# Kernel optimization log

Hardware: AMD Instinct MI355X
Metric: run time of the kernel (lower is better)

Reference implementation:

```python
import jax, jax.numpy as jnp
import numpy as np

B, CTX, DIMS, HEAD = 8, 4096, 1024, 16
HD = DIMS // HEAD
EPS = 1e-5
THRESH = 0.01   # self.threshold.item()
FACTOR = 0.1    # self.factor.item()
MAX_IT = 3


def setup_inputs() -> dict:
    key = jax.random.key(0)
    ks = jax.random.split(key, 9)
    w = lambda k, shp: jax.random.normal(k, shp, jnp.float32) * 0.02
    return {
        "x": jax.random.normal(ks[0], (B, CTX, DIMS), jnp.float32),
        "qw": w(ks[1], (DIMS, DIMS)), "qb": jnp.zeros((DIMS,), jnp.float32),
        "kw": w(ks[2], (DIMS, DIMS)),  # k linear has bias=False
        "vw": w(ks[3], (DIMS, DIMS)), "vb": jnp.zeros((DIMS,), jnp.float32),
        "ow": w(ks[4], (DIMS, DIMS)), "ob": jnp.zeros((DIMS,), jnp.float32),
        "lna_w": jnp.ones((DIMS,), jnp.float32),
        "lnb_w": jnp.ones((DIMS,), jnp.float32),
        "lnc_w": jnp.ones((HD,), jnp.float32),
        "lnd_w": jnp.ones((HD,), jnp.float32),
        "lqw": w(ks[5], (HD, HD)), "lqb": jnp.zeros((HD,), jnp.float32),
        "lkw": w(ks[6], (HD, HD)), "lkb": jnp.zeros((HD,), jnp.float32),
        "lvw": w(ks[7], (HD, HD)), "lvb": jnp.zeros((HD,), jnp.float32),
    }


def _ln(x, w):
    # torch LayerNorm with bias=False (biased variance)
    m = jnp.mean(x, axis=-1, keepdims=True)
    v = jnp.mean((x - m) ** 2, axis=-1, keepdims=True)
    return (x - m) * jax.lax.rsqrt(v + EPS) * w


def reference(x, qw, qb, kw, vw, vb, ow, ob, lna_w, lnb_w, lnc_w, lnd_w,
              lqw, lqb, lkw, lkb, lvw, lvb):
    b, ctx, dims = x.shape
    q = _ln(x, lna_w) @ qw.T + qb
    xb = _ln(x, lnb_w)
    k = xb @ kw.T
    v = xb @ vw.T + vb
    split = lambda t: t.reshape(b, ctx, HEAD, HD).transpose(0, 2, 1, 3)  # [b,h,s,d]
    query, key_t, value = split(q), split(k), split(v)

    # Faithful to source bug: eff_span = min(seq, qcur.size(1)=head, key.size(1)=head)
    eff = min(ctx, HEAD)

    # key/value side of the inner loop is iteration-invariant -> compute once
    kn = _ln(key_t[:, :, :eff, :] @ lkw.T + lkb, lnd_w)
    vi = value[:, :, :eff, :] @ lvw.T + lvb
    scale = 1.0 / np.sqrt(HD)

    def step(qcur):
        qn = _ln(qcur[:, :, :eff, :] @ lqw.T + lqb, lnc_w)
        logits = jnp.einsum('bhqd,bhkd->bhqk', qn, kn) * scale
        attn = jax.nn.softmax(logits, axis=-1) @ vi  # is_causal=False (mask is None)
        return jnp.zeros_like(qcur).at[:, :, :eff, :].set(attn)

    prev = jnp.zeros_like(query)
    attn_out = jnp.zeros_like(query)
    qcur = query
    done = jnp.asarray(False)
    for it in range(MAX_IT):
        iter_out = step(qcur)
        diff = jnp.mean(jnp.abs(iter_out - prev))
        brk = (diff < THRESH + FACTOR * diff) & jnp.asarray(it > 0) & (~done)
        attn_out = jnp.where(done, attn_out, iter_out)
        prev = jnp.where(done, prev, iter_out)
        qcur = jnp.where(done | brk, qcur, qcur + iter_out)
        done = done | brk

    out = attn_out.transpose(0, 2, 1, 3).reshape(b, ctx, dims)
    return out @ ow.T + ob
```

## Files before the change

kernel.cpp:

```cpp
#include <hip/hip_runtime.h>

typedef unsigned short u16;
typedef __attribute__((ext_vector_type(8))) short short8;
typedef __attribute__((ext_vector_type(4))) float f32x4;

#define LSTR 68

__device__ __forceinline__ u16 f2bf(float f){
  union { float f; unsigned int i; } v; v.f = f;
  unsigned int x = v.i;
  return (u16)((x + 0x7FFFu + ((x >> 16) & 1u)) >> 16);
}

__device__ __forceinline__ short8 cvt8(const float* __restrict__ p){
  float4 a = *(const float4*)p;
  float4 b = *(const float4*)(p + 4);
  short8 r;
  r[0]=(short)f2bf(a.x); r[1]=(short)f2bf(a.y); r[2]=(short)f2bf(a.z); r[3]=(short)f2bf(a.w);
  r[4]=(short)f2bf(b.x); r[5]=(short)f2bf(b.y); r[6]=(short)f2bf(b.z); r[7]=(short)f2bf(b.w);
  return r;
}

__global__ __launch_bounds__(256) void k_ln(const float* __restrict__ x,
    const float* __restrict__ lna, const float* __restrict__ lnb,
    u16* __restrict__ xa, u16* __restrict__ xb)
{
  __shared__ float ssum[4], ssq[4];
  int row = blockIdx.x;
  int b = row >> 4, s = row & 15;
  int tid = threadIdx.x;
  const float* xr = x + ((size_t)b*4096 + s)*1024;
  float4 v = *(const float4*)(xr + tid*4);
  float sum = v.x+v.y+v.z+v.w;
  float sq  = v.x*v.x+v.y*v.y+v.z*v.z+v.w*v.w;
  #pragma unroll
  for (int o=32;o>0;o>>=1){ sum += __shfl_xor(sum,o); sq += __shfl_xor(sq,o); }
  int w = tid>>6;
  if ((tid&63)==0){ ssum[w]=sum; ssq[w]=sq; }
  __syncthreads();
  sum = ssum[0]+ssum[1]+ssum[2]+ssum[3];
  sq  = ssq[0]+ssq[1]+ssq[2]+ssq[3];
  float m   = sum * (1.f/1024.f);
  float var = sq  * (1.f/1024.f) - m*m;
  float rs  = rsqrtf(fmaxf(var, 0.f) + 1e-5f);
  float4 wa = *(const float4*)(lna + tid*4);
  float4 wb = *(const float4*)(lnb + tid*4);
  float n0=(v.x-m)*rs, n1=(v.y-m)*rs, n2=(v.z-m)*rs, n3=(v.w-m)*rs;
  ushort4 oa, obv;
  oa.x=f2bf(n0*wa.x); oa.y=f2bf(n1*wa.y); oa.z=f2bf(n2*wa.z); oa.w=f2bf(n3*wa.w);
  obv.x=f2bf(n0*wb.x); obv.y=f2bf(n1*wb.y); obv.z=f2bf(n2*wb.z); obv.w=f2bf(n3*wb.w);
  *(ushort4*)(xa + (size_t)row*1024 + tid*4) = oa;
  *(ushort4*)(xb + (size_t)row*1024 + tid*4) = obv;
}

__global__ __launch_bounds__(256) void k_proj(const u16* __restrict__ xa, const u16* __restrict__ xb,
    const float* __restrict__ qw, const float* __restrict__ qb,
    const float* __restrict__ kw, const float* __restrict__ vw, const float* __restrict__ vb,
    float* __restrict__ qkv)
{
  int tid = threadIdx.x, wave = tid>>6, lane = tid&63;
  int tile = blockIdx.x*4 + wave;
  int mt = tile / 192, nt = tile % 192;
  int mat = nt >> 6, nct = nt & 63;
  const u16*   A = (mat==0) ? xa : xb;
  const float* W = (mat==0) ? qw : ((mat==1) ? kw : vw);
  int m_lane = lane & 15, quad = lane >> 4;
  const u16*   ap = A + (size_t)(mt*16  + m_lane)*1024 + quad*8;
  const float* bp = W + (size_t)(nct*16 + m_lane)*1024 + quad*8;
  f32x4 acc = {0.f,0.f,0.f,0.f};
  #pragma unroll 4
  for (int k0=0;k0<1024;k0+=32){
    short8 af = *(const short8*)(ap + k0);
    short8 bf = cvt8(bp + k0);
    acc = __builtin_amdgcn_mfma_f32_16x16x32_bf16(af, bf, acc, 0, 0, 0);
  }
  int n = nct*16 + m_lane;
  float bias = 0.f;
  if (mat==0) bias = qb[n];
  else if (mat==2) bias = vb[n];
  float* outp = qkv + (size_t)mat*131072;
  #pragma unroll
  for (int i=0;i<4;i++){
    int row = mt*16 + quad*4 + i;
    outp[(size_t)row*1024 + n] = acc[i] + bias;
  }
}

__device__ __forceinline__ void mm4(const float* __restrict__ X, const float* __restrict__ W,
                                    const float* __restrict__ bias, int r, int cg, float out4[4])
{
  const float* xrow = X + r*LSTR;
  #pragma unroll
  for (int i=0;i<4;i++){
    int o = cg*4+i;
    const float* wrow = W + o*LSTR;
    float acc = bias[o];
    #pragma unroll
    for (int d=0; d<64; d+=4){
      float4 w4 = *(const float4*)(wrow + d);
      float4 x4 = *(const float4*)(xrow + d);
      acc += x4.x*w4.x + x4.y*w4.y + x4.z*w4.z + x4.w*w4.w;
    }
    out4[i] = acc;
  }
}

__device__ __forceinline__ void ln4(float v[4], const float* __restrict__ lnw, int cg)
{
  float s = v[0]+v[1]+v[2]+v[3];
  float q = v[0]*v[0]+v[1]*v[1]+v[2]*v[2]+v[3]*v[3];
  #pragma unroll
  for (int m=1;m<16;m<<=1){ s += __shfl_xor(s,m); q += __shfl_xor(q,m); }
  float mn  = s * (1.f/64.f);
  float var = q * (1.f/64.f) - mn*mn;
  float rs  = rsqrtf(fmaxf(var,0.f) + 1e-5f);
  #pragma unroll
  for (int i=0;i<4;i++) v[i] = (v[i]-mn)*rs*lnw[cg*4+i];
}

__device__ __forceinline__ void attn_iter(const float* __restrict__ qsrc,
    const float* __restrict__ wq, const float* __restrict__ lqb, const float* __restrict__ lnc,
    float* __restrict__ qns, float* __restrict__ ps,
    const float* __restrict__ kks, const float* __restrict__ vis,
    int r, int cg, float a4[4])
{
  int c0 = cg*4;
  float qn4[4];
  mm4(qsrc, wq, lqb, r, cg, qn4);
  ln4(qn4, lnc, cg);
  #pragma unroll
  for (int i=0;i<4;i++) qns[r*LSTR+c0+i] = qn4[i];
  __syncthreads();
  float acc = 0.f;
  #pragma unroll
  for (int d=0;d<64;d+=4){
    float4 a = *(const float4*)(qns + r*LSTR + d);
    float4 b = *(const float4*)(kks + cg*LSTR + d);
    acc += a.x*b.x + a.y*b.y + a.z*b.z + a.w*b.w;
  }
  acc *= 0.125f;
  float mx = acc;
  #pragma unroll
  for (int m=1;m<16;m<<=1) mx = fmaxf(mx, __shfl_xor(mx,m));
  float e = __expf(acc - mx);
  float sm = e;
  #pragma unroll
  for (int m=1;m<16;m<<=1) sm += __shfl_xor(sm,m);
  ps[r*17+cg] = e / sm;
  __syncthreads();
  #pragma unroll
  for (int i=0;i<4;i++){
    int o = c0+i; float s = 0.f;
    #pragma unroll
    for (int c=0;c<16;c++) s += ps[r*17+c]*vis[c*LSTR+o];
    a4[i] = s;
  }
}

__global__ __launch_bounds__(256) void k_attn(const float* __restrict__ qkv,
    const float* __restrict__ lnc, const float* __restrict__ lnd,
    const float* __restrict__ lqw, const float* __restrict__ lqb,
    const float* __restrict__ lkw, const float* __restrict__ lkb,
    const float* __restrict__ lvw, const float* __restrict__ lvb,
    u16* __restrict__ attn)
{
  __shared__ float qs[16*LSTR], ks[16*LSTR], vs[16*LSTR];
  __shared__ float kks[16*LSTR], vis[16*LSTR], qns[16*LSTR], qcs[16*LSTR];
  __shared__ float ps[16*17];
  __shared__ float wq[64*LSTR], wk[64*LSTR], wv[64*LSTR];
  __shared__ float sb[5*64];

  int tid = threadIdx.x, bh = blockIdx.x;
  int b = bh>>4, h = bh&15;
  int r = tid>>4, cg = tid&15, c0 = cg*4;

  for (int i = tid; i < 1024; i += 256){
    int o = i >> 4, d = (i & 15)*4;
    *(float4*)(wq + o*LSTR + d) = *(const float4*)(lqw + i*4);
    *(float4*)(wk + o*LSTR + d) = *(const float4*)(lkw + i*4);
    *(float4*)(wv + o*LSTR + d) = *(const float4*)(lvw + i*4);
  }
  if (tid < 64){
    sb[tid]       = lqb[tid];
    sb[64  + tid] = lkb[tid];
    sb[128 + tid] = lvb[tid];
    sb[192 + tid] = lnc[tid];
    sb[256 + tid] = lnd[tid];
  }
  size_t base = (size_t)(b*16 + r)*1024 + h*64 + c0;
  float4 fq = *(const float4*)(qkv + base);
  float4 fk = *(const float4*)(qkv + 131072 + base);
  float4 fv = *(const float4*)(qkv + 262144 + base);
  float q4[4] = {fq.x, fq.y, fq.z, fq.w};
  #pragma unroll
  for (int i=0;i<4;i++) qs[r*LSTR+c0+i] = q4[i];
  *(float4*)(ks + r*LSTR + c0) = fk;
  *(float4*)(vs + r*LSTR + c0) = fv;
  __syncthreads();

  float kk4[4]; mm4(ks, wk, sb+64, r, cg, kk4); ln4(kk4, sb+256, cg);
  float vi4[4]; mm4(vs, wv, sb+128, r, cg, vi4);
  #pragma unroll
  for (int i=0;i<4;i++){ kks[r*LSTR+c0+i] = kk4[i]; vis[r*LSTR+c0+i] = vi4[i]; }
  __syncthreads();

  float a4[4];
  attn_iter(qs, wq, sb+0, sb+192, qns, ps, kks, vis, r, cg, a4);
  #pragma unroll
  for (int i=0;i<4;i++) qcs[r*LSTR+c0+i] = q4[i] + a4[i];
  __syncthreads();
  attn_iter(qcs, wq, sb+0, sb+192, qns, ps, kks, vis, r, cg, a4);

  ushort4 ov;
  ov.x=f2bf(a4[0]); ov.y=f2bf(a4[1]); ov.z=f2bf(a4[2]); ov.w=f2bf(a4[3]);
  *(ushort4*)(attn + (size_t)(b*16 + r)*1024 + h*64 + c0) = ov;
}

__global__ __launch_bounds__(256) void k_fill(const float* __restrict__ ob, float* __restrict__ out)
{
  size_t idx = ((size_t)blockIdx.x*256 + threadIdx.x)*4;
  int o = (int)(idx & 1023);
  *(float4*)(out + idx) = *(const float4*)(ob + o);
}

__global__ __launch_bounds__(256) void k_oproj(const u16* __restrict__ attn,
    const float* __restrict__ ow, const float* __restrict__ ob, float* __restrict__ out)
{
  int tid = threadIdx.x, wave = tid>>6, lane = tid&63;
  int tile = blockIdx.x*4 + wave;
  int mt = tile >> 6, nt = tile & 63;
  int m_lane = lane & 15, quad = lane >> 4;
  const u16*   ap = attn + (size_t)(mt*16 + m_lane)*1024 + quad*8;
  const float* bp = ow   + (size_t)(nt*16 + m_lane)*1024 + quad*8;
  f32x4 acc = {0.f,0.f,0.f,0.f};
  #pragma unroll 4
  for (int k0=0;k0<1024;k0+=32){
    short8 af = *(const short8*)(ap + k0);
    short8 bf = cvt8(bp + k0);
    acc = __builtin_amdgcn_mfma_f32_16x16x32_bf16(af, bf, acc, 0, 0, 0);
  }
  int n = nt*16 + m_lane;
  float bias = ob[n];
  #pragma unroll
  for (int i=0;i<4;i++){
    int s = quad*4 + i;
    out[((size_t)mt*4096 + s)*1024 + n] = acc[i] + bias;
  }
}

extern "C" void kernel_launch(void* const* d_in, const int* in_sizes, int n_in,
                              void* d_out, int out_size, void* d_ws, size_t ws_size,
                              hipStream_t stream)
{
  const float* x    = (const float*)d_in[0];
  const float* qw   = (const float*)d_in[1];
  const float* qb   = (const float*)d_in[2];
  const float* kw   = (const float*)d_in[3];
  const float* vw   = (const float*)d_in[4];
  const float* vb   = (const float*)d_in[5];
  const float* ow   = (const float*)d_in[6];
  const float* ob   = (const float*)d_in[7];
  const float* lna  = (const float*)d_in[8];
  const float* lnb  = (const float*)d_in[9];
  const float* lnc  = (const float*)d_in[10];
  const float* lnd  = (const float*)d_in[11];
  const float* lqw  = (const float*)d_in[12];
  const float* lqb  = (const float*)d_in[13];
  const float* lkw  = (const float*)d_in[14];
  const float* lkb  = (const float*)d_in[15];
  const float* lvw  = (const float*)d_in[16];
  const float* lvb  = (const float*)d_in[17];

  char* ws = (char*)d_ws;
  u16*   xa   = (u16*)(ws);
  u16*   xb   = (u16*)(ws + 262144);
  float* qkv  = (float*)(ws + 524288);
  u16*   attn = (u16*)(ws + 2097152);
  float* out  = (float*)d_out;

  k_ln   <<<  128, 256, 0, stream>>>(x, lna, lnb, xa, xb);
  k_proj <<<  384, 256, 0, stream>>>(xa, xb, qw, qb, kw, vw, vb, qkv);
  k_attn <<<  128, 256, 0, stream>>>(qkv, lnc, lnd, lqw, lqb, lkw, lkb, lvw, lvb, attn);
  k_fill <<<32768, 256, 0, stream>>>(ob, out);
  k_oproj<<<  128, 256, 0, stream>>>(attn, ow, ob, out);
}
```

Measured before the change: 285.0 us.

## Fuse layernorm into QKV projection and bias fill into output projection

Merges the layernorm kernel into the QKV projection: each block recomputes LN for its 16 rows into LDS and feeds MFMA from shared memory, which removes the global xa/xb round trip and one launch. Merges the bias broadcast fill and the output projection into one grid, with fill blocks skipping the 16 rows that the projection writes. This cuts two kernel launches and some redundant writes. The cost is that LN is recomputed 48 times per row group and LDS use per block rises.

```diff
diff --git a/kernel.cpp b/kernel.cpp
--- a/kernel.cpp
+++ b/kernel.cpp
@@ -5,6 +5,7 @@
 typedef __attribute__((ext_vector_type(4))) float f32x4;
 
 #define LSTR 68
+#define ASTR 1032
 
 __device__ __forceinline__ u16 f2bf(float f){
   union { float f; unsigned int i; } v; v.f = f;
@@ -21,51 +22,54 @@
   return r;
 }
 
-__global__ __launch_bounds__(256) void k_ln(const float* __restrict__ x,
+__global__ __launch_bounds__(256) void k_lnproj(const float* __restrict__ x,
     const float* __restrict__ lna, const float* __restrict__ lnb,
-    u16* __restrict__ xa, u16* __restrict__ xb)
-{
-  __shared__ float ssum[4], ssq[4];
-  int row = blockIdx.x;
-  int b = row >> 4, s = row & 15;
-  int tid = threadIdx.x;
-  const float* xr = x + ((size_t)b*4096 + s)*1024;
-  float4 v = *(const float4*)(xr + tid*4);
-  float sum = v.x+v.y+v.z+v.w;
-  float sq  = v.x*v.x+v.y*v.y+v.z*v.z+v.w*v.w;
-  #pragma unroll
-  for (int o=32;o>0;o>>=1){ sum += __shfl_xor(sum,o); sq += __shfl_xor(sq,o); }
-  int w = tid>>6;
-  if ((tid&63)==0){ ssum[w]=sum; ssq[w]=sq; }
-  __syncthreads();
-  sum = ssum[0]+ssum[1]+ssum[2]+ssum[3];
-  sq  = ssq[0]+ssq[1]+ssq[2]+ssq[3];
-  float m   = sum * (1.f/1024.f);
-  float var = sq  * (1.f/1024.f) - m*m;
+    const float* __restrict__ qw, const float* __restrict__ qb,
+    const float* __restrict__ kw, const float* __restrict__ vw,
+    const float* __restrict__ vb, float* __restrict__ qkv)
+{
+  __shared__ u16 Aa[16*ASTR];
+  __shared__ u16 Ab[16*ASTR];
+
+  int tid = threadIdx.x, wave = tid>>6, lane = tid&63;
+  int blk = blockIdx.x;
+  int mt  = blk / 48;
+
+  int r = tid >> 4, l16 = tid & 15;
+  const float* xr = x + ((size_t)mt*4096 + r)*1024;
+  float4 vv[16];
+  float sum = 0.f, sq = 0.f;
+  #pragma unroll
+  for (int j=0;j<16;j++){
+    vv[j] = *(const float4*)(xr + (j*16 + l16)*4);
+    sum += vv[j].x+vv[j].y+vv[j].z+vv[j].w;
+    sq  += vv[j].x*vv[j].x + vv[j].y*vv[j].y + vv[j].z*vv[j].z + vv[j].w*vv[j].w;
+  }
+  #pragma unroll
+  for (int m=1;m<16;m<<=1){ sum += __shfl_xor(sum,m); sq += __shfl_xor(sq,m); }
+  float mn  = sum * (1.f/1024.f);
+  float var = sq  * (1.f/1024.f) - mn*mn;
   float rs  = rsqrtf(fmaxf(var, 0.f) + 1e-5f);
-  float4 wa = *(const float4*)(lna + tid*4);
-  float4 wb = *(const float4*)(lnb + tid*4);
-  float n0=(v.x-m)*rs, n1=(v.y-m)*rs, n2=(v.z-m)*rs, n3=(v.w-m)*rs;
-  ushort4 oa, obv;
-  oa.x=f2bf(n0*wa.x); oa.y=f2bf(n1*wa.y); oa.z=f2bf(n2*wa.z); oa.w=f2bf(n3*wa.w);
-  obv.x=f2bf(n0*wb.x); obv.y=f2bf(n1*wb.y); obv.z=f2bf(n2*wb.z); obv.w=f2bf(n3*wb.w);
-  *(ushort4*)(xa + (size_t)row*1024 + tid*4) = oa;
-  *(ushort4*)(xb + (size_t)row*1024 + tid*4) = obv;
-}
-
-__global__ __launch_bounds__(256) void k_proj(const u16* __restrict__ xa, const u16* __restrict__ xb,
-    const float* __restrict__ qw, const float* __restrict__ qb,
-    const float* __restrict__ kw, const float* __restrict__ vw, const float* __restrict__ vb,
-    float* __restrict__ qkv)
-{
-  int tid = threadIdx.x, wave = tid>>6, lane = tid&63;
-  int tile = blockIdx.x*4 + wave;
-  int mt = tile / 192, nt = tile % 192;
-  int mat = nt >> 6, nct = nt & 63;
-  const u16*   A = (mat==0) ? xa : xb;
-  const float* W = (mat==0) ? qw : ((mat==1) ? kw : vw);
+  #pragma unroll
+  for (int j=0;j<16;j++){
+    int c = (j*16 + l16)*4;
+    float4 wa = *(const float4*)(lna + c);
+    float4 wb = *(const float4*)(lnb + c);
+    float n0=(vv[j].x-mn)*rs, n1=(vv[j].y-mn)*rs, n2=(vv[j].z-mn)*rs, n3=(vv[j].w-mn)*rs;
+    ushort4 oa, obv;
+    oa.x =f2bf(n0*wa.x); oa.y =f2bf(n1*wa.y); oa.z =f2bf(n2*wa.z); oa.w =f2bf(n3*wa.w);
+    obv.x=f2bf(n0*wb.x); obv.y=f2bf(n1*wb.y); obv.z=f2bf(n2*wb.z); obv.w=f2bf(n3*wb.w);
+    *(ushort4*)(Aa + r*ASTR + c) = oa;
+    *(ushort4*)(Ab + r*ASTR + c) = obv;
+  }
+  __syncthreads();
+
+  int tile = blk*4 + wave;
+  int nt = tile % 192, mat = nt >> 6, nct = nt & 63;
+  const u16*   Al = (mat==0) ? Aa : Ab;
+  const float* W  = (mat==0) ? qw : ((mat==1) ? kw : vw);
   int m_lane = lane & 15, quad = lane >> 4;
-  const u16*   ap = A + (size_t)(mt*16  + m_lane)*1024 + quad*8;
+  const u16*   ap = Al + m_lane*ASTR + quad*8;
   const float* bp = W + (size_t)(nct*16 + m_lane)*1024 + quad*8;
   f32x4 acc = {0.f,0.f,0.f,0.f};
   #pragma unroll 4
@@ -216,18 +220,18 @@
   *(ushort4*)(attn + (size_t)(b*16 + r)*1024 + h*64 + c0) = ov;
 }
 
-__global__ __launch_bounds__(256) void k_fill(const float* __restrict__ ob, float* __restrict__ out)
-{
-  size_t idx = ((size_t)blockIdx.x*256 + threadIdx.x)*4;
-  int o = (int)(idx & 1023);
-  *(float4*)(out + idx) = *(const float4*)(ob + o);
-}
-
-__global__ __launch_bounds__(256) void k_oproj(const u16* __restrict__ attn,
+__global__ __launch_bounds__(256) void k_fillproj(const u16* __restrict__ attn,
     const float* __restrict__ ow, const float* __restrict__ ob, float* __restrict__ out)
 {
-  int tid = threadIdx.x, wave = tid>>6, lane = tid&63;
-  int tile = blockIdx.x*4 + wave;
+  int tid = threadIdx.x;
+  if (blockIdx.x < 32768){
+    int row = blockIdx.x;
+    if ((row & 4095) < 16) return;
+    *(float4*)(out + (size_t)row*1024 + tid*4) = *(const float4*)(ob + tid*4);
+    return;
+  }
+  int wave = tid>>6, lane = tid&63;
+  int tile = (blockIdx.x - 32768)*4 + wave;
   int mt = tile >> 6, nt = tile & 63;
   int m_lane = lane & 15, quad = lane >> 4;
   const u16*   ap = attn + (size_t)(mt*16 + m_lane)*1024 + quad*8;
@@ -272,15 +276,11 @@
   const float* lvb  = (const float*)d_in[17];
 
   char* ws = (char*)d_ws;
-  u16*   xa   = (u16*)(ws);
-  u16*   xb   = (u16*)(ws + 262144);
-  float* qkv  = (float*)(ws + 524288);
-  u16*   attn = (u16*)(ws + 2097152);
+  float* qkv  = (float*)(ws);
+  u16*   attn = (u16*)(ws + 1572864);
   float* out  = (float*)d_out;
 
-  k_ln   <<<  128, 256, 0, stream>>>(x, lna, lnb, xa, xb);
-  k_proj <<<  384, 256, 0, stream>>>(xa, xb, qw, qb, kw, vw, vb, qkv);
-  k_attn <<<  128, 256, 0, stream>>>(qkv, lnc, lnd, lqw, lqb, lkw, lkb, lvw, lvb, attn);
-  k_fill <<<32768, 256, 0, stream>>>(ob, out);
-  k_oproj<<<  128, 256, 0, stream>>>(attn, ow, ob, out);
-}
+  k_lnproj  <<<  384, 256, 0, stream>>>(x, lna, lnb, qw, qb, kw, vw, vb, qkv);
+  k_attn    <<<  128, 256, 0, stream>>>(qkv, lnc, lnd, lqw, lqb, lkw, lkb, lvw, lvb, attn);
+  k_fillproj<<<32896, 256, 0, stream>>>(attn, ow, ob, out);
+}
```

After: 283.5 us. About the same (-0.5%).
